# Optimization experiments

Hardware: AMD Instinct MI355X
Metric: run time of the kernel (lower is better)

The kernel has to match this reference:

```python
import jax, jax.numpy as jnp
import numpy as np

N, D, R, NUM_HEADS = 8192, 256, 32, 4
ETA = 0.5


def setup_inputs() -> dict:
    key = jax.random.key(0)
    k_h, k_a, k_u = jax.random.split(key, 3)
    H = jax.random.normal(k_h, (N, D), dtype=jnp.float32)
    # sparse-ish symmetric adjacency with self loops (float mask, as in torch code)
    A = (jax.random.uniform(k_a, (N, N)) < 0.002).astype(jnp.float32)
    A = jnp.maximum(jnp.maximum(A, A.T), jnp.eye(N, dtype=jnp.float32))
    # symmetric normalized Laplacian L = I - D^{-1/2} A D^{-1/2}
    dinv = 1.0 / jnp.sqrt(A.sum(axis=1))
    L = jnp.eye(N, dtype=jnp.float32) - dinv[:, None] * A * dinv[None, :]
    # per-head orthonormal subspace bases U[k] in R^{D x R} (QR init as in module)
    raw = jax.random.normal(k_u, (NUM_HEADS, D, R), dtype=jnp.float32)
    U = jnp.linalg.qr(raw)[0]  # batched reduced QR -> [K, D, R]
    lambda_lap = jnp.asarray(0.1, dtype=jnp.float32)
    threshold = jnp.full((D,), 0.05, dtype=jnp.float32)
    return {"H": H, "adj_mask": A, "L": L, "U": U,
            "lambda_lap": lambda_lap, "threshold": threshold}


def reference(H, adj_mask, L, U, lambda_lap, threshold):
    n, d = H.shape
    K, _, r = U.shape
    scale = 1.0 / (r ** 0.5)
    neg = (1.0 - adj_mask) * -1e9  # additive graph mask, shared across heads

    Ht = H.T  # [d, n]
    agg = jnp.zeros_like(Ht)
    for k in range(K):  # small fixed head loop (keeps one [n,n] block live at a time)
        Uk = U[k]                      # [d, r]
        Zk = Uk.T @ Ht                 # [r, n]
        scores = (Zk.T @ Zk) * scale + neg  # [n, n]
        alpha = jax.nn.softmax(scores, axis=1)
        agg = agg + Uk @ (Zk @ alpha.T)     # [d, n]

    lap_grad = lambda_lap * (L @ H)        # [n, d]
    H_half = (Ht + ETA * agg).T - ETA * lap_grad
    # proximal soft-threshold (proj is None since in_dim == out_dim)
    H_out = jnp.sign(H_half) * jax.nn.relu(jnp.abs(H_half) - threshold[None, :])

    # orthogonality regularizer over all head pairs
    G = jnp.einsum('kdr,lds->klrs', U, U)  # [K, K, r, r] (small)
    I = jnp.eye(r, dtype=U.dtype)
    diag_loss = ((G[jnp.arange(K), jnp.arange(K)] - I) ** 2).sum()
    upper = jnp.triu(jnp.ones((K, K), dtype=U.dtype), 1)
    off_loss = ((G ** 2).sum(axis=(2, 3)) * upper).sum()
    orth_loss = diag_loss + off_loss

    lap_smooth = jnp.sum(H_out * (L @ H_out))  # trace(H_out^T L H_out)
    return H_out, orth_loss, lap_smooth
```

## Files before the change

### kernel.cpp

```cpp
#include <hip/hip_runtime.h>
#include <hip/hip_bf16.h>
#include <math.h>

#define NN 8192
#define DD 256
#define RR 32
#define KH 4
#define PP 128
#define CAP 128
#define CAPL 128
#define NSTASH 48
#define ETA 0.5f
#define SCALE 0.17677669529663687f

__device__ __forceinline__ unsigned short f2bf(float f) {
  union { float f; unsigned u; } v; v.f = f;
  unsigned r = v.u + 0x7fffu + ((v.u >> 16) & 1u);
  return (unsigned short)(r >> 16);
}
__device__ __forceinline__ float bflo(unsigned u) { return __uint_as_float(u << 16); }
__device__ __forceinline__ float bfhi(unsigned u) { return __uint_as_float(u & 0xffff0000u); }

__global__ __launch_bounds__(256) void zgemm_scan(const float* __restrict__ A,
                                                  const float* __restrict__ H,
                                                  const float* __restrict__ U,
                                                  float* __restrict__ B2,
                                                  unsigned short* __restrict__ Zb,
                                                  unsigned short* __restrict__ Hb,
                                                  float* __restrict__ orth_part,
                                                  int* __restrict__ lowCols,
                                                  int* __restrict__ lowCnt,
                                                  int* __restrict__ upCols,
                                                  int* __restrict__ upCnt) {
  __shared__ float smem[5152];
  int tid = threadIdx.x;
  int bx = blockIdx.x;
  int lane = tid & 63, wv = tid >> 6;

  if (bx >= 650) {
    int row = (NN - 1) - (bx - 650);
    const float* a = A + (size_t)row * NN;
    __shared__ int wsum2[4];
    __shared__ int sbase;
    if (tid == 0) sbase = 0;
    int nch = (row >> 10) + 1;
    for (int c = 0; c < nch; ++c) {
      int g0 = c * 1024 + tid * 4;
      float4 x = *(const float4*)(a + g0);
      int m0 = (g0 + 0 < row) && (x.x != 0.f);
      int m1 = (g0 + 1 < row) && (x.y != 0.f);
      int m2 = (g0 + 2 < row) && (x.z != 0.f);
      int m3 = (g0 + 3 < row) && (x.w != 0.f);
      int cnt = m0 + m1 + m2 + m3;
      int incl = cnt;
#pragma unroll
      for (int off = 1; off < 64; off <<= 1) {
        int t = __shfl_up(incl, off);
        if (lane >= off) incl += t;
      }
      if (lane == 63) wsum2[wv] = incl;
      __syncthreads();
      int base = sbase;
#pragma unroll
      for (int w = 0; w < 4; ++w) if (w < wv) base += wsum2[w];
      int o = base + incl - cnt;
      int chunkTot = wsum2[0] + wsum2[1] + wsum2[2] + wsum2[3];
      if (m0) { int col = g0 + 0; if (o < CAPL) { lowCols[(size_t)row * CAPL + o] = col; int s = atomicAdd(&upCnt[col], 1); if (s < CAPL) upCols[(size_t)col * CAPL + s] = row; } o++; }
      if (m1) { int col = g0 + 1; if (o < CAPL) { lowCols[(size_t)row * CAPL + o] = col; int s = atomicAdd(&upCnt[col], 1); if (s < CAPL) upCols[(size_t)col * CAPL + s] = row; } o++; }
      if (m2) { int col = g0 + 2; if (o < CAPL) { lowCols[(size_t)row * CAPL + o] = col; int s = atomicAdd(&upCnt[col], 1); if (s < CAPL) upCols[(size_t)col * CAPL + s] = row; } o++; }
      if (m3) { int col = g0 + 3; if (o < CAPL) { lowCols[(size_t)row * CAPL + o] = col; int s = atomicAdd(&upCnt[col], 1); if (s < CAPL) upCols[(size_t)col * CAPL + s] = row; } o++; }
      __syncthreads();
      if (tid == 0) sbase = base + chunkTot;
    }
    __syncthreads();
    if (tid == 0) lowCnt[row] = sbase;
    return;
  }
  if (bx >= 394) {
    int base = (bx - 394) * 8192;
#pragma unroll
    for (int q = 0; q < 8; ++q) {
      int idx = base + q * 1024 + tid * 4;
      float4 v = *(const float4*)(H + idx);
      uint2 p;
      p.x = (unsigned)f2bf(v.x) | ((unsigned)f2bf(v.y) << 16);
      p.y = (unsigned)f2bf(v.z) | ((unsigned)f2bf(v.w) << 16);
      *(uint2*)(Hb + idx) = p;
    }
    return;
  }
  if (bx >= 266) {
    int idx = (bx - 266) * 256 + tid;
    int k = idx / (DD * RR);
    int rem = idx % (DD * RR);
    int d = rem / RR;
    int r = rem % RR;
    B2[(k * RR + r) * DD + d] = U[idx];
    return;
  }
  if (bx >= 256) {
    int bid = bx - 256;
    int b = bid, k = 0;
    while (b >= (KH - k)) { b -= (KH - k); k++; }
    int l = k + b;
    float* redo = smem;
    const float* uk = U + (size_t)k * DD * RR;
    const float* ul = U + (size_t)l * DD * RR;
    float acc = 0.f;
#pragma unroll
    for (int q = 0; q < 4; ++q) {
      int e = tid * 4 + q;
      int r = e >> 5, s2 = e & 31;
      float g = 0.f;
      for (int d = 0; d < DD; ++d) g += uk[d * RR + r] * ul[d * RR + s2];
      if (k == l) {
        float c3 = g - (r == s2 ? 1.f : 0.f);
        acc += c3 * c3;
      } else {
        acc += g * g;
      }
    }
    redo[tid] = acc;
    __syncthreads();
    for (int off = 128; off > 0; off >>= 1) {
      if (tid < off) redo[tid] += redo[tid + off];
      __syncthreads();
    }
    if (tid == 0) orth_part[bid] = redo[0];
    return;
  }
  float* As = smem;
  float* Bs = smem + 1056;
  int r0 = bx * 32;
  int tx = tid & 15, ty = tid >> 4;
  int cx = tx * 8, ry = ty * 2;
  float acc[2][8];
#pragma unroll
  for (int i = 0; i < 2; ++i)
#pragma unroll
    for (int j = 0; j < 8; ++j) acc[i][j] = 0.f;

  for (int k0 = 0; k0 < DD; k0 += 32) {
    {
      int r = tid >> 3;
      int kc = (tid & 7) * 4;
      float4 x = *(const float4*)(H + (size_t)(r0 + r) * DD + k0 + kc);
      As[(kc + 0) * 33 + r] = x.x; As[(kc + 1) * 33 + r] = x.y;
      As[(kc + 2) * 33 + r] = x.z; As[(kc + 3) * 33 + r] = x.w;
    }
#pragma unroll
    for (int q = 0; q < 4; ++q) {
      int f = tid + 256 * q;
      int kk = f >> 5, pc = (f & 31) * 4;
      *(float4*)(&Bs[kk * 128 + pc]) =
          *(const float4*)(U + (size_t)(pc >> 5) * DD * RR + (size_t)(k0 + kk) * RR + (pc & 31));
    }
    __syncthreads();
#pragma unroll
    for (int kk = 0; kk < 32; ++kk) {
      float av[2];
      av[0] = As[kk * 33 + ry]; av[1] = As[kk * 33 + ry + 1];
      float bv[8];
      *(float4*)(bv) = *(const float4*)(&Bs[kk * 128 + cx]);
      *(float4*)(bv + 4) = *(const float4*)(&Bs[kk * 128 + cx + 4]);
#pragma unroll
      for (int i = 0; i < 2; ++i)
#pragma unroll
        for (int j = 0; j < 8; ++j) acc[i][j] += av[i] * bv[j];
    }
    __syncthreads();
  }
#pragma unroll
  for (int i = 0; i < 2; ++i) {
    uint4 p;
    p.x = (unsigned)f2bf(acc[i][0]) | ((unsigned)f2bf(acc[i][1]) << 16);
    p.y = (unsigned)f2bf(acc[i][2]) | ((unsigned)f2bf(acc[i][3]) << 16);
    p.z = (unsigned)f2bf(acc[i][4]) | ((unsigned)f2bf(acc[i][5]) << 16);
    p.w = (unsigned)f2bf(acc[i][6]) | ((unsigned)f2bf(acc[i][7]) << 16);
    *(uint4*)(Zb + (size_t)(r0 + ry + i) * PP + cx) = p;
  }
}

__global__ __launch_bounds__(256) void csr_attn_s(const unsigned short* __restrict__ Zb,
                                                  const unsigned short* __restrict__ Hb,
                                                  const int* __restrict__ lowCols,
                                                  const int* __restrict__ lowCnt,
                                                  const int* __restrict__ upCols,
                                                  const int* __restrict__ upCnt,
                                                  float* __restrict__ dinv,
                                                  float* __restrict__ aggZ,
                                                  float* __restrict__ S) {
  int row = blockIdx.x;
  int tid = threadIdx.x;
  int lane = tid & 63, wv = tid >> 6;
  __shared__ int scols[CAP];
  __shared__ int utmp[CAPL];
  __shared__ float zi[PP];
  __shared__ unsigned short zzb[NSTASH][130];
  __shared__ float sdinv[CAP];
  __shared__ float uni[1024];

  if (tid < PP) zi[tid] = bflo((unsigned)Zb[(size_t)row * PP + tid]);

  int lcT = lowCnt[row];
  int ucT = upCnt[row];
  int lc = lcT < (CAP - 1) ? lcT : (CAP - 1);
  for (int t = tid; t < lc; t += 256) scols[t] = lowCols[(size_t)row * CAPL + t];
  if (tid == 0) scols[lc] = row;
  int ucR = ucT < CAPL ? ucT : CAPL;
  for (int t = tid; t < ucR; t += 256) utmp[t] = upCols[(size_t)row * CAPL + t];
  __syncthreads();
  for (int t = tid; t < ucR; t += 256) {
    int e = utmp[t], r = 0;
    for (int q = 0; q < ucR; ++q) r += (utmp[q] < e);
    int pos = lc + 1 + r;
    if (pos < CAP) scols[pos] = e;
  }
  int total = lcT + 1 + ucT;
  int nn = total < CAP ? total : CAP;
  if (tid == 0) dinv[row] = 1.0f / sqrtf((float)total);
  __syncthreads();

  if (tid < nn) {
    int c = scols[tid];
    int cc = lowCnt[c] + 1 + upCnt[c];
    sdinv[tid] = 1.0f / sqrtf((float)cc);
  }
  __syncthreads();

  {
    float4 acc = make_float4(0.f, 0.f, 0.f, 0.f);
    for (int jj = wv; jj < nn; jj += 4) {
      int c = scols[jj];
      if (jj < NSTASH) {
        unsigned x = *(const unsigned*)(Zb + (size_t)c * PP + lane * 2);
        *(unsigned*)(&zzb[jj][lane * 2]) = x;
      }
      uint2 u = *(const uint2*)(Hb + (size_t)c * DD + lane * 4);
      float w = sdinv[jj];
      acc.x += w * bflo(u.x); acc.y += w * bfhi(u.x);
      acc.z += w * bflo(u.y); acc.w += w * bfhi(u.y);
    }
    *(float4*)(&uni[wv * 256 + lane * 4]) = acc;
  }
  __syncthreads();
  {
    float s = uni[0 * 256 + tid] + uni[1 * 256 + tid] + uni[2 * 256 + tid] + uni[3 * 256 + tid];
    S[(size_t)row * DD + tid] = s;
  }
  __syncthreads();

  {
    int k = wv;
    float s0 = -1e30f, s1 = -1e30f;
    if (lane < nn) {
      float acc = 0.f;
      if (lane < NSTASH) {
        const unsigned short* zs = &zzb[lane][k * RR];
#pragma unroll
        for (int r = 0; r < RR; r += 4) {
          float4 aa = *(const float4*)(zi + k * RR + r);
          unsigned u0 = *(const unsigned*)(zs + r);
          unsigned u1 = *(const unsigned*)(zs + r + 2);
          acc += aa.x * bflo(u0) + aa.y * bfhi(u0) + aa.z * bflo(u1) + aa.w * bfhi(u1);
        }
      } else {
        const unsigned short* zj = Zb + (size_t)scols[lane] * PP + k * RR;
#pragma unroll
        for (int r = 0; r < RR; r += 4) {
          float4 aa = *(const float4*)(zi + k * RR + r);
          unsigned u0 = *(const unsigned*)(zj + r);
          unsigned u1 = *(const unsigned*)(zj + r + 2);
          acc += aa.x * bflo(u0) + aa.y * bfhi(u0) + aa.z * bflo(u1) + aa.w * bfhi(u1);
        }
      }
      s0 = acc * SCALE;
    }
    int j1 = lane + 64;
    if (j1 < nn) {
      const unsigned short* zj = Zb + (size_t)scols[j1] * PP + k * RR;
      float acc = 0.f;
#pragma unroll
      for (int r = 0; r < RR; r += 4) {
        float4 aa = *(const float4*)(zi + k * RR + r);
        unsigned u0 = *(const unsigned*)(zj + r);
        unsigned u1 = *(const unsigned*)(zj + r + 2);
        acc += aa.x * bflo(u0) + aa.y * bfhi(u0) + aa.z * bflo(u1) + aa.w * bfhi(u1);
      }
      s1 = acc * SCALE;
    }
    float m = fmaxf(s0, s1);
#pragma unroll
    for (int off = 32; off > 0; off >>= 1) m = fmaxf(m, __shfl_xor(m, off));
    float e0 = (lane < nn) ? expf(s0 - m) : 0.f;
    float e1 = (j1 < nn) ? expf(s1 - m) : 0.f;
    float s = e0 + e1;
#pragma unroll
    for (int off = 32; off > 0; off >>= 1) s += __shfl_xor(s, off);
    float inv = 1.0f / s;
    if (lane < nn) uni[k * CAP + lane] = e0 * inv;
    if (j1 < nn) uni[k * CAP + j1] = e1 * inv;
  }
  __syncthreads();

  {
    int c2 = tid & 63, hf = tid >> 6;
    int hd = c2 >> 4;
    float a0 = 0.f, a1 = 0.f;
    for (int jj = hf; jj < nn; jj += 4) {
      unsigned u;
      if (jj < NSTASH) u = *(const unsigned*)(&zzb[jj][c2 * 2]);
      else u = *(const unsigned*)(Zb + (size_t)scols[jj] * PP + c2 * 2);
      float al = uni[hd * CAP + jj];
      a0 += al * bflo(u);
      a1 += al * bfhi(u);
    }
    *(float2*)(&uni[512 + hf * 128 + c2 * 2]) = make_float2(a0, a1);
  }
  __syncthreads();
  if (tid < 64) {
    float2 r0 = *(float2*)(&uni[512 + 0 * 128 + tid * 2]);
    float2 r1 = *(float2*)(&uni[512 + 1 * 128 + tid * 2]);
    float2 r2 = *(float2*)(&uni[512 + 2 * 128 + tid * 2]);
    float2 r3 = *(float2*)(&uni[512 + 3 * 128 + tid * 2]);
    float2 s2 = make_float2(r0.x + r1.x + r2.x + r3.x, r0.y + r1.y + r2.y + r3.y);
    *(float2*)(aggZ + (size_t)row * PP + tid * 2) = s2;
  }
}

__global__ __launch_bounds__(256) void egemm(const float* __restrict__ A,
                                             const float* __restrict__ B,
                                             const float* __restrict__ Hm,
                                             const float* __restrict__ S,
                                             const float* __restrict__ dinv,
                                             const float* __restrict__ thr,
                                             const float* __restrict__ lambda_p,
                                             float* __restrict__ out,
                                             unsigned short* __restrict__ Houtb) {
  __shared__ float As[32][33];
  __shared__ float Bs[32][128];
  int tid = threadIdx.x;
  int r0 = blockIdx.x * 32;
  int c0 = blockIdx.y * 128;
  int tx = tid & 15, ty = tid >> 4;
  int cx = tx * 8, ry = ty * 2;
  float acc[2][8];
#pragma unroll
  for (int i = 0; i < 2; ++i)
#pragma unroll
    for (int j = 0; j < 8; ++j) acc[i][j] = 0.f;

  for (int k0 = 0; k0 < PP; k0 += 32) {
    {
      int r = tid >> 3;
      int kc = (tid & 7) * 4;
      float4 x = *(const float4*)(A + (size_t)(r0 + r) * PP + k0 + kc);
      As[kc + 0][r] = x.x; As[kc + 1][r] = x.y; As[kc + 2][r] = x.z; As[kc + 3][r] = x.w;
    }
#pragma unroll
    for (int q = 0; q < 4; ++q) {
      int f = tid + 256 * q;
      int kk = f >> 5, pc = (f & 31) * 4;
      *(float4*)(&Bs[kk][pc]) = *(const float4*)(B + (size_t)(k0 + kk) * DD + c0 + pc);
    }
    __syncthreads();
#pragma unroll
    for (int kk = 0; kk < 32; ++kk) {
      float av[2];
      av[0] = As[kk][ry]; av[1] = As[kk][ry + 1];
      float bv[8];
      *(float4*)(bv) = *(const float4*)(&Bs[kk][cx]);
      *(float4*)(bv + 4) = *(const float4*)(&Bs[kk][cx + 4]);
#pragma unroll
      for (int i = 0; i < 2; ++i)
#pragma unroll
        for (int j = 0; j < 8; ++j) acc[i][j] += av[i] * bv[j];
    }
    __syncthreads();
  }
  float lam = lambda_p[0];
  int gc = c0 + cx;
  float4 t0 = *(const float4*)(thr + gc);
  float4 t1 = *(const float4*)(thr + gc + 4);
#pragma unroll
  for (int i = 0; i < 2; ++i) {
    int gr = r0 + ry + i;
    float dv = dinv[gr];
    float4 h0 = *(const float4*)(Hm + (size_t)gr * DD + gc);
    float4 h1 = *(const float4*)(Hm + (size_t)gr * DD + gc + 4);
    float4 s0 = *(const float4*)(S + (size_t)gr * DD + gc);
    float4 s1 = *(const float4*)(S + (size_t)gr * DD + gc + 4);
    float hv[8] = {h0.x, h0.y, h0.z, h0.w, h1.x, h1.y, h1.z, h1.w};
    float sv[8] = {s0.x, s0.y, s0.z, s0.w, s1.x, s1.y, s1.z, s1.w};
    float tv[8] = {t0.x, t0.y, t0.z, t0.w, t1.x, t1.y, t1.z, t1.w};
    float ov[8];
#pragma unroll
    for (int j = 0; j < 8; ++j) {
      float val = hv[j] + ETA * acc[i][j] - ETA * lam * (hv[j] - dv * sv[j]);
      float av = fabsf(val) - tv[j];
      ov[j] = (av > 0.f) ? copysignf(av, val) : 0.f;
    }
    *(float4*)(out + (size_t)gr * DD + gc) = make_float4(ov[0], ov[1], ov[2], ov[3]);
    *(float4*)(out + (size_t)gr * DD + gc + 4) = make_float4(ov[4], ov[5], ov[6], ov[7]);
    uint4 p;
    p.x = (unsigned)f2bf(ov[0]) | ((unsigned)f2bf(ov[1]) << 16);
    p.y = (unsigned)f2bf(ov[2]) | ((unsigned)f2bf(ov[3]) << 16);
    p.z = (unsigned)f2bf(ov[4]) | ((unsigned)f2bf(ov[5]) << 16);
    p.w = (unsigned)f2bf(ov[6]) | ((unsigned)f2bf(ov[7]) << 16);
    *(uint4*)(Houtb + (size_t)gr * DD + gc) = p;
  }
}

__global__ __launch_bounds__(256) void lap_rows(const float* __restrict__ Hout,
                                                const unsigned short* __restrict__ Houtb,
                                                const int* __restrict__ lowCols,
                                                const int* __restrict__ lowCnt,
                                                const float* __restrict__ dinv,
                                                float* __restrict__ part) {
  int row = (NN - 1) - blockIdx.x;
  int tid = threadIdx.x;
  int lane = tid & 63, wv = tid >> 6;
  __shared__ int scols[CAPL];
  __shared__ float sdinv[CAPL];
  __shared__ float sred[4][260];
  int lcT = lowCnt[row];
  int lc = lcT < CAPL ? lcT : CAPL;
  if (tid < lc) {
    int c = lowCols[(size_t)row * CAPL + tid];
    scols[tid] = c;
    sdinv[tid] = 2.0f * dinv[c];
  }
  __syncthreads();
  float4 acc = make_float4(0.f, 0.f, 0.f, 0.f);
  for (int jj = wv; jj < lc; jj += 4) {
    uint2 u = *(const uint2*)(Houtb + (size_t)scols[jj] * DD + lane * 4);
    float w = sdinv[jj];
    acc.x += w * bflo(u.x); acc.y += w * bfhi(u.x);
    acc.z += w * bflo(u.y); acc.w += w * bfhi(u.y);
  }
  *(float4*)(&sred[wv][lane * 4]) = acc;
  __syncthreads();
  if (wv == 0) {
    float4 s4;
    s4.x = sred[0][lane * 4 + 0] + sred[1][lane * 4 + 0] + sred[2][lane * 4 + 0] + sred[3][lane * 4 + 0];
    s4.y = sred[0][lane * 4 + 1] + sred[1][lane * 4 + 1] + sred[2][lane * 4 + 1] + sred[3][lane * 4 + 1];
    s4.z = sred[0][lane * 4 + 2] + sred[1][lane * 4 + 2] + sred[2][lane * 4 + 2] + sred[3][lane * 4 + 2];
    s4.w = sred[0][lane * 4 + 3] + sred[1][lane * 4 + 3] + sred[2][lane * 4 + 3] + sred[3][lane * 4 + 3];
    float4 h4 = *(const float4*)(Hout + (size_t)row * DD + lane * 4);
    float dvr = dinv[row];
    float own = 1.0f - dvr * dvr;
    float val = h4.x * (own * h4.x - dvr * s4.x) + h4.y * (own * h4.y - dvr * s4.y) +
                h4.z * (own * h4.z - dvr * s4.z) + h4.w * (own * h4.w - dvr * s4.w);
#pragma unroll
    for (int off = 32; off > 0; off >>= 1) val += __shfl_xor(val, off);
    if (lane == 0) part[row] = val;
  }
}

__global__ __launch_bounds__(256) void finalize(const float* __restrict__ lap_part,
                                                const float* __restrict__ orth_part,
                                                float* __restrict__ out) {
  __shared__ double red[256];
  int tid = threadIdx.x;
  double s = 0.0;
  for (int i = tid; i < NN; i += 256) s += (double)lap_part[i];
  red[tid] = s;
  __syncthreads();
  for (int off = 128; off > 0; off >>= 1) {
    if (tid < off) red[tid] += red[tid + off];
    __syncthreads();
  }
  if (tid == 0) {
    double o = 0.0;
    for (int i = 0; i < 10; ++i) o += (double)orth_part[i];
    out[(size_t)NN * DD] = (float)o;
    out[(size_t)NN * DD + 1] = (float)red[0];
  }
}

extern "C" void kernel_launch(void* const* d_in, const int* in_sizes, int n_in,
                              void* d_out, int out_size, void* d_ws, size_t ws_size,
                              hipStream_t stream) {
  const float* H = (const float*)d_in[0];
  const float* A = (const float*)d_in[1];
  const float* U = (const float*)d_in[3];
  const float* lambda_p = (const float*)d_in[4];
  const float* thr = (const float*)d_in[5];
  float* out = (float*)d_out;

  char* w = (char*)d_ws;
  float* B2 = (float*)w;             w += (size_t)PP * DD * 4;
  int* lowCols = (int*)w;            w += (size_t)NN * CAPL * 4;
  int* upCols = (int*)w;             w += (size_t)NN * CAPL * 4;
  int* lowCnt = (int*)w;             w += (size_t)NN * 4;
  int* upCnt = (int*)w;              w += (size_t)NN * 4;
  float* dinv = (float*)w;           w += (size_t)NN * 4;
  unsigned short* Zb = (unsigned short*)w;   w += (size_t)NN * PP * 2;
  unsigned short* Hb = (unsigned short*)w;   w += (size_t)NN * DD * 2;
  unsigned short* Houtb = (unsigned short*)w; w += (size_t)NN * DD * 2;
  float* aggZ = (float*)w;           w += (size_t)NN * PP * 4;
  float* S = (float*)w;              w += (size_t)NN * DD * 4;
  float* lap_part = (float*)w;       w += (size_t)NN * 4;
  float* orth_part = (float*)w;      w += 64;

  hipMemsetAsync(upCnt, 0, (size_t)NN * 4, stream);
  zgemm_scan<<<dim3(650 + NN), dim3(256), 0, stream>>>(A, H, U, B2, Zb, Hb, orth_part,
                                                       lowCols, lowCnt, upCols, upCnt);
  csr_attn_s<<<dim3(NN), dim3(256), 0, stream>>>(Zb, Hb, lowCols, lowCnt, upCols, upCnt,
                                                 dinv, aggZ, S);
  egemm<<<dim3(NN / 32, 2), dim3(256), 0, stream>>>(aggZ, B2, H, S, dinv, thr, lambda_p,
                                                    out, Houtb);
  lap_rows<<<dim3(NN), dim3(256), 0, stream>>>(out, Houtb, lowCols, lowCnt, dinv, lap_part);
  finalize<<<dim3(1), dim3(256), 0, stream>>>(lap_part, orth_part, out);
}
```

Measured before the change: 152.6 us.

## Fuse sparse Laplacian gather into epilogue GEMM, drop S intermediate

The weighted neighbor sum of bf16 H (the L@H term) moves out of the attention kernel and into the egemm kernel. The attention kernel now writes a compact per-row column list and nnz count, and egemm gathers each 32-row by 128-column tile into shared memory before its GEMM loop. This removes the full-size fp32 S buffer write and re-read. In exchange, the gather now runs in a grid of only 512 blocks issuing small 4-byte loads, so latency may be less well hidden, and a new cols array is written.

```diff
diff --git a/kernel.cpp b/kernel.cpp
--- a/kernel.cpp
+++ b/kernel.cpp
@@ -181,15 +181,15 @@
   }
 }
 
-__global__ __launch_bounds__(256) void csr_attn_s(const unsigned short* __restrict__ Zb,
-                                                  const unsigned short* __restrict__ Hb,
-                                                  const int* __restrict__ lowCols,
-                                                  const int* __restrict__ lowCnt,
-                                                  const int* __restrict__ upCols,
-                                                  const int* __restrict__ upCnt,
-                                                  float* __restrict__ dinv,
-                                                  float* __restrict__ aggZ,
-                                                  float* __restrict__ S) {
+__global__ __launch_bounds__(256) void csr_attn(const unsigned short* __restrict__ Zb,
+                                                const int* __restrict__ lowCols,
+                                                const int* __restrict__ lowCnt,
+                                                const int* __restrict__ upCols,
+                                                const int* __restrict__ upCnt,
+                                                int* __restrict__ cols,
+                                                int* __restrict__ nnzArr,
+                                                float* __restrict__ dinv,
+                                                float* __restrict__ aggZ) {
   int row = blockIdx.x;
   int tid = threadIdx.x;
   int lane = tid & 63, wv = tid >> 6;
@@ -197,7 +197,6 @@
   __shared__ int utmp[CAPL];
   __shared__ float zi[PP];
   __shared__ unsigned short zzb[NSTASH][130];
-  __shared__ float sdinv[CAP];
   __shared__ float uni[1024];
 
   if (tid < PP) zi[tid] = bflo((unsigned)Zb[(size_t)row * PP + tid]);
@@ -219,34 +218,14 @@
   int total = lcT + 1 + ucT;
   int nn = total < CAP ? total : CAP;
   if (tid == 0) dinv[row] = 1.0f / sqrtf((float)total);
-  __syncthreads();
-
-  if (tid < nn) {
-    int c = scols[tid];
-    int cc = lowCnt[c] + 1 + upCnt[c];
-    sdinv[tid] = 1.0f / sqrtf((float)cc);
-  }
-  __syncthreads();
-
-  {
-    float4 acc = make_float4(0.f, 0.f, 0.f, 0.f);
-    for (int jj = wv; jj < nn; jj += 4) {
-      int c = scols[jj];
-      if (jj < NSTASH) {
-        unsigned x = *(const unsigned*)(Zb + (size_t)c * PP + lane * 2);
-        *(unsigned*)(&zzb[jj][lane * 2]) = x;
-      }
-      uint2 u = *(const uint2*)(Hb + (size_t)c * DD + lane * 4);
-      float w = sdinv[jj];
-      acc.x += w * bflo(u.x); acc.y += w * bfhi(u.x);
-      acc.z += w * bflo(u.y); acc.w += w * bfhi(u.y);
-    }
-    *(float4*)(&uni[wv * 256 + lane * 4]) = acc;
-  }
-  __syncthreads();
-  {
-    float s = uni[0 * 256 + tid] + uni[1 * 256 + tid] + uni[2 * 256 + tid] + uni[3 * 256 + tid];
-    S[(size_t)row * DD + tid] = s;
+  if (tid == 0) nnzArr[row] = nn;
+  __syncthreads();
+  for (int t = tid; t < nn; t += 256) cols[(size_t)row * CAP + t] = scols[t];
+
+  int ns = nn < NSTASH ? nn : NSTASH;
+  for (int j = wv; j < ns; j += 4) {
+    unsigned x = *(const unsigned*)(Zb + (size_t)scols[j] * PP + lane * 2);
+    *(unsigned*)(&zzb[j][lane * 2]) = x;
   }
   __syncthreads();
 
@@ -331,7 +310,9 @@
 __global__ __launch_bounds__(256) void egemm(const float* __restrict__ A,
                                              const float* __restrict__ B,
                                              const float* __restrict__ Hm,
-                                             const float* __restrict__ S,
+                                             const unsigned short* __restrict__ Hb,
+                                             const int* __restrict__ cols,
+                                             const int* __restrict__ nnzArr,
                                              const float* __restrict__ dinv,
                                              const float* __restrict__ thr,
                                              const float* __restrict__ lambda_p,
@@ -339,11 +320,38 @@
                                              unsigned short* __restrict__ Houtb) {
   __shared__ float As[32][33];
   __shared__ float Bs[32][128];
+  __shared__ float Stile[32][130];
   int tid = threadIdx.x;
+  int lane = tid & 63, wv = tid >> 6;
   int r0 = blockIdx.x * 32;
   int c0 = blockIdx.y * 128;
   int tx = tid & 15, ty = tid >> 4;
   int cx = tx * 8, ry = ty * 2;
+
+  for (int r = wv; r < 32; r += 4) {
+    int gr = r0 + r;
+    int nn = nnzArr[gr];
+    const int* cp = cols + (size_t)gr * CAP;
+    float a0 = 0.f, a1 = 0.f, b0 = 0.f, b1 = 0.f;
+    int jj = 0;
+    for (; jj + 1 < nn; jj += 2) {
+      int ca = cp[jj], cb = cp[jj + 1];
+      float wa = dinv[ca], wb = dinv[cb];
+      unsigned ua = *(const unsigned*)(Hb + (size_t)ca * DD + c0 + lane * 2);
+      unsigned ub = *(const unsigned*)(Hb + (size_t)cb * DD + c0 + lane * 2);
+      a0 += wa * bflo(ua); a1 += wa * bfhi(ua);
+      b0 += wb * bflo(ub); b1 += wb * bfhi(ub);
+    }
+    if (jj < nn) {
+      int ca = cp[jj];
+      float wa = dinv[ca];
+      unsigned ua = *(const unsigned*)(Hb + (size_t)ca * DD + c0 + lane * 2);
+      a0 += wa * bflo(ua); a1 += wa * bfhi(ua);
+    }
+    Stile[r][lane * 2] = a0 + b0;
+    Stile[r][lane * 2 + 1] = a1 + b1;
+  }
+
   float acc[2][8];
 #pragma unroll
   for (int i = 0; i < 2; ++i)
@@ -378,6 +386,7 @@
     }
     __syncthreads();
   }
+
   float lam = lambda_p[0];
   int gc = c0 + cx;
   float4 t0 = *(const float4*)(thr + gc);
@@ -388,15 +397,13 @@
     float dv = dinv[gr];
     float4 h0 = *(const float4*)(Hm + (size_t)gr * DD + gc);
     float4 h1 = *(const float4*)(Hm + (size_t)gr * DD + gc + 4);
-    float4 s0 = *(const float4*)(S + (size_t)gr * DD + gc);
-    float4 s1 = *(const float4*)(S + (size_t)gr * DD + gc + 4);
     float hv[8] = {h0.x, h0.y, h0.z, h0.w, h1.x, h1.y, h1.z, h1.w};
-    float sv[8] = {s0.x, s0.y, s0.z, s0.w, s1.x, s1.y, s1.z, s1.w};
     float tv[8] = {t0.x, t0.y, t0.z, t0.w, t1.x, t1.y, t1.z, t1.w};
     float ov[8];
 #pragma unroll
     for (int j = 0; j < 8; ++j) {
-      float val = hv[j] + ETA * acc[i][j] - ETA * lam * (hv[j] - dv * sv[j]);
+      float sv = Stile[ry + i][cx + j];
+      float val = hv[j] + ETA * acc[i][j] - ETA * lam * (hv[j] - dv * sv);
       float av = fabsf(val) - tv[j];
       ov[j] = (av > 0.f) ? copysignf(av, val) : 0.f;
     }
@@ -492,24 +499,25 @@
   float* B2 = (float*)w;             w += (size_t)PP * DD * 4;
   int* lowCols = (int*)w;            w += (size_t)NN * CAPL * 4;
   int* upCols = (int*)w;             w += (size_t)NN * CAPL * 4;
+  int* cols = (int*)w;               w += (size_t)NN * CAP * 4;
   int* lowCnt = (int*)w;             w += (size_t)NN * 4;
   int* upCnt = (int*)w;              w += (size_t)NN * 4;
+  int* nnzArr = (int*)w;             w += (size_t)NN * 4;
   float* dinv = (float*)w;           w += (size_t)NN * 4;
   unsigned short* Zb = (unsigned short*)w;   w += (size_t)NN * PP * 2;
   unsigned short* Hb = (unsigned short*)w;   w += (size_t)NN * DD * 2;
   unsigned short* Houtb = (unsigned short*)w; w += (size_t)NN * DD * 2;
   float* aggZ = (float*)w;           w += (size_t)NN * PP * 4;
-  float* S = (float*)w;              w += (size_t)NN * DD * 4;
   float* lap_part = (float*)w;       w += (size_t)NN * 4;
   float* orth_part = (float*)w;      w += 64;
 
   hipMemsetAsync(upCnt, 0, (size_t)NN * 4, stream);
   zgemm_scan<<<dim3(650 + NN), dim3(256), 0, stream>>>(A, H, U, B2, Zb, Hb, orth_part,
                                                        lowCols, lowCnt, upCols, upCnt);
-  csr_attn_s<<<dim3(NN), dim3(256), 0, stream>>>(Zb, Hb, lowCols, lowCnt, upCols, upCnt,
-                                                 dinv, aggZ, S);
-  egemm<<<dim3(NN / 32, 2), dim3(256), 0, stream>>>(aggZ, B2, H, S, dinv, thr, lambda_p,
-                                                    out, Houtb);
+  csr_attn<<<dim3(NN), dim3(256), 0, stream>>>(Zb, lowCols, lowCnt, upCols, upCnt,
+                                               cols, nnzArr, dinv, aggZ);
+  egemm<<<dim3(NN / 32, 2), dim3(256), 0, stream>>>(aggZ, B2, H, Hb, cols, nnzArr, dinv,
+                                                    thr, lambda_p, out, Houtb);
   lap_rows<<<dim3(NN), dim3(256), 0, stream>>>(out, Houtb, lowCols, lowCnt, dinv, lap_part);
   finalize<<<dim3(1), dim3(256), 0, stream>>>(lap_part, orth_part, out);
 }
```

Result: slower. 197.1 us (+29.1%).

## Fuse output GEMM and epilogue into per-row sparse attention kernel

Applied to the files above, without the earlier changes.

Removes the separate egemm kernel. Each row block of the attention kernel now multiplies its aggregated Z vector by a bf16 copy of the U basis (B2b) and applies the Laplacian-gradient and soft-threshold epilogue itself. This avoids writing and re-reading the aggZ and S intermediates and saves a kernel launch. In exchange, each block re-reads the 64KB bf16 basis from cache as a per-row matrix-vector product, and U is now rounded to bf16.

```diff
diff --git a/kernel.cpp b/kernel.cpp
--- a/kernel.cpp
+++ b/kernel.cpp
@@ -24,7 +24,7 @@
 __global__ __launch_bounds__(256) void zgemm_scan(const float* __restrict__ A,
                                                   const float* __restrict__ H,
                                                   const float* __restrict__ U,
-                                                  float* __restrict__ B2,
+                                                  unsigned short* __restrict__ B2b,
                                                   unsigned short* __restrict__ Zb,
                                                   unsigned short* __restrict__ Hb,
                                                   float* __restrict__ orth_part,
@@ -95,7 +95,7 @@
     int rem = idx % (DD * RR);
     int d = rem / RR;
     int r = rem % RR;
-    B2[(k * RR + r) * DD + d] = U[idx];
+    B2b[(k * RR + r) * DD + d] = f2bf(U[idx]);
     return;
   }
   if (bx >= 256) {
@@ -181,15 +181,19 @@
   }
 }
 
-__global__ __launch_bounds__(256) void csr_attn_s(const unsigned short* __restrict__ Zb,
-                                                  const unsigned short* __restrict__ Hb,
-                                                  const int* __restrict__ lowCols,
-                                                  const int* __restrict__ lowCnt,
-                                                  const int* __restrict__ upCols,
-                                                  const int* __restrict__ upCnt,
-                                                  float* __restrict__ dinv,
-                                                  float* __restrict__ aggZ,
-                                                  float* __restrict__ S) {
+__global__ __launch_bounds__(256) void csr_attn_full(const unsigned short* __restrict__ Zb,
+                                                     const unsigned short* __restrict__ Hb,
+                                                     const unsigned short* __restrict__ B2b,
+                                                     const float* __restrict__ Hm,
+                                                     const float* __restrict__ thr,
+                                                     const float* __restrict__ lambda_p,
+                                                     const int* __restrict__ lowCols,
+                                                     const int* __restrict__ lowCnt,
+                                                     const int* __restrict__ upCols,
+                                                     const int* __restrict__ upCnt,
+                                                     float* __restrict__ dinv,
+                                                     float* __restrict__ out,
+                                                     unsigned short* __restrict__ Houtb) {
   int row = blockIdx.x;
   int tid = threadIdx.x;
   int lane = tid & 63, wv = tid >> 6;
@@ -218,7 +222,8 @@
   }
   int total = lcT + 1 + ucT;
   int nn = total < CAP ? total : CAP;
-  if (tid == 0) dinv[row] = 1.0f / sqrtf((float)total);
+  float dvRow = 1.0f / sqrtf((float)total);
+  if (tid == 0) dinv[row] = dvRow;
   __syncthreads();
 
   if (tid < nn) {
@@ -244,10 +249,7 @@
     *(float4*)(&uni[wv * 256 + lane * 4]) = acc;
   }
   __syncthreads();
-  {
-    float s = uni[0 * 256 + tid] + uni[1 * 256 + tid] + uni[2 * 256 + tid] + uni[3 * 256 + tid];
-    S[(size_t)row * DD + tid] = s;
-  }
+  float sReg = uni[0 * 256 + tid] + uni[1 * 256 + tid] + uni[2 * 256 + tid] + uni[3 * 256 + tid];
   __syncthreads();
 
   {
@@ -323,91 +325,37 @@
     float2 r1 = *(float2*)(&uni[512 + 1 * 128 + tid * 2]);
     float2 r2 = *(float2*)(&uni[512 + 2 * 128 + tid * 2]);
     float2 r3 = *(float2*)(&uni[512 + 3 * 128 + tid * 2]);
-    float2 s2 = make_float2(r0.x + r1.x + r2.x + r3.x, r0.y + r1.y + r2.y + r3.y);
-    *(float2*)(aggZ + (size_t)row * PP + tid * 2) = s2;
-  }
-}
-
-__global__ __launch_bounds__(256) void egemm(const float* __restrict__ A,
-                                             const float* __restrict__ B,
-                                             const float* __restrict__ Hm,
-                                             const float* __restrict__ S,
-                                             const float* __restrict__ dinv,
-                                             const float* __restrict__ thr,
-                                             const float* __restrict__ lambda_p,
-                                             float* __restrict__ out,
-                                             unsigned short* __restrict__ Houtb) {
-  __shared__ float As[32][33];
-  __shared__ float Bs[32][128];
-  int tid = threadIdx.x;
-  int r0 = blockIdx.x * 32;
-  int c0 = blockIdx.y * 128;
-  int tx = tid & 15, ty = tid >> 4;
-  int cx = tx * 8, ry = ty * 2;
-  float acc[2][8];
-#pragma unroll
-  for (int i = 0; i < 2; ++i)
-#pragma unroll
-    for (int j = 0; j < 8; ++j) acc[i][j] = 0.f;
-
-  for (int k0 = 0; k0 < PP; k0 += 32) {
-    {
-      int r = tid >> 3;
-      int kc = (tid & 7) * 4;
-      float4 x = *(const float4*)(A + (size_t)(r0 + r) * PP + k0 + kc);
-      As[kc + 0][r] = x.x; As[kc + 1][r] = x.y; As[kc + 2][r] = x.z; As[kc + 3][r] = x.w;
-    }
-#pragma unroll
-    for (int q = 0; q < 4; ++q) {
-      int f = tid + 256 * q;
-      int kk = f >> 5, pc = (f & 31) * 4;
-      *(float4*)(&Bs[kk][pc]) = *(const float4*)(B + (size_t)(k0 + kk) * DD + c0 + pc);
-    }
-    __syncthreads();
-#pragma unroll
-    for (int kk = 0; kk < 32; ++kk) {
-      float av[2];
-      av[0] = As[kk][ry]; av[1] = As[kk][ry + 1];
-      float bv[8];
-      *(float4*)(bv) = *(const float4*)(&Bs[kk][cx]);
-      *(float4*)(bv + 4) = *(const float4*)(&Bs[kk][cx + 4]);
-#pragma unroll
-      for (int i = 0; i < 2; ++i)
-#pragma unroll
-        for (int j = 0; j < 8; ++j) acc[i][j] += av[i] * bv[j];
-    }
-    __syncthreads();
-  }
-  float lam = lambda_p[0];
-  int gc = c0 + cx;
-  float4 t0 = *(const float4*)(thr + gc);
-  float4 t1 = *(const float4*)(thr + gc + 4);
-#pragma unroll
-  for (int i = 0; i < 2; ++i) {
-    int gr = r0 + ry + i;
-    float dv = dinv[gr];
-    float4 h0 = *(const float4*)(Hm + (size_t)gr * DD + gc);
-    float4 h1 = *(const float4*)(Hm + (size_t)gr * DD + gc + 4);
-    float4 s0 = *(const float4*)(S + (size_t)gr * DD + gc);
-    float4 s1 = *(const float4*)(S + (size_t)gr * DD + gc + 4);
-    float hv[8] = {h0.x, h0.y, h0.z, h0.w, h1.x, h1.y, h1.z, h1.w};
-    float sv[8] = {s0.x, s0.y, s0.z, s0.w, s1.x, s1.y, s1.z, s1.w};
-    float tv[8] = {t0.x, t0.y, t0.z, t0.w, t1.x, t1.y, t1.z, t1.w};
-    float ov[8];
-#pragma unroll
-    for (int j = 0; j < 8; ++j) {
-      float val = hv[j] + ETA * acc[i][j] - ETA * lam * (hv[j] - dv * sv[j]);
-      float av = fabsf(val) - tv[j];
-      ov[j] = (av > 0.f) ? copysignf(av, val) : 0.f;
-    }
-    *(float4*)(out + (size_t)gr * DD + gc) = make_float4(ov[0], ov[1], ov[2], ov[3]);
-    *(float4*)(out + (size_t)gr * DD + gc + 4) = make_float4(ov[4], ov[5], ov[6], ov[7]);
-    uint4 p;
-    p.x = (unsigned)f2bf(ov[0]) | ((unsigned)f2bf(ov[1]) << 16);
-    p.y = (unsigned)f2bf(ov[2]) | ((unsigned)f2bf(ov[3]) << 16);
-    p.z = (unsigned)f2bf(ov[4]) | ((unsigned)f2bf(ov[5]) << 16);
-    p.w = (unsigned)f2bf(ov[6]) | ((unsigned)f2bf(ov[7]) << 16);
-    *(uint4*)(Houtb + (size_t)gr * DD + gc) = p;
+    uni[tid * 2] = r0.x + r1.x + r2.x + r3.x;
+    uni[tid * 2 + 1] = r0.y + r1.y + r2.y + r3.y;
+  }
+  __syncthreads();
+
+  {
+    int g = tid >> 7, t = tid & 127;
+    float a0 = 0.f, a1 = 0.f;
+    int pbase = g * 64;
+#pragma unroll 8
+    for (int p = 0; p < 64; ++p) {
+      float az = uni[pbase + p];
+      unsigned u = *(const unsigned*)(B2b + (size_t)(pbase + p) * DD + t * 2);
+      a0 += az * bflo(u);
+      a1 += az * bfhi(u);
+    }
+    uni[512 + g * 256 + t * 2] = a0;
+    uni[512 + g * 256 + t * 2 + 1] = a1;
+  }
+  __syncthreads();
+
+  {
+    float agg = uni[512 + tid] + uni[768 + tid];
+    float h = Hm[(size_t)row * DD + tid];
+    float lam = lambda_p[0];
+    float t = thr[tid];
+    float val = h + ETA * agg - ETA * lam * (h - dvRow * sReg);
+    float av = fabsf(val) - t;
+    float ov = (av > 0.f) ? copysignf(av, val) : 0.f;
+    out[(size_t)row * DD + tid] = ov;
+    Houtb[(size_t)row * DD + tid] = f2bf(ov);
   }
 }
 
@@ -489,7 +437,7 @@
   float* out = (float*)d_out;
 
   char* w = (char*)d_ws;
-  float* B2 = (float*)w;             w += (size_t)PP * DD * 4;
+  unsigned short* B2b = (unsigned short*)w;  w += (size_t)PP * DD * 2;
   int* lowCols = (int*)w;            w += (size_t)NN * CAPL * 4;
   int* upCols = (int*)w;             w += (size_t)NN * CAPL * 4;
   int* lowCnt = (int*)w;             w += (size_t)NN * 4;
@@ -498,18 +446,15 @@
   unsigned short* Zb = (unsigned short*)w;   w += (size_t)NN * PP * 2;
   unsigned short* Hb = (unsigned short*)w;   w += (size_t)NN * DD * 2;
   unsigned short* Houtb = (unsigned short*)w; w += (size_t)NN * DD * 2;
-  float* aggZ = (float*)w;           w += (size_t)NN * PP * 4;
-  float* S = (float*)w;              w += (size_t)NN * DD * 4;
   float* lap_part = (float*)w;       w += (size_t)NN * 4;
   float* orth_part = (float*)w;      w += 64;
 
   hipMemsetAsync(upCnt, 0, (size_t)NN * 4, stream);
-  zgemm_scan<<<dim3(650 + NN), dim3(256), 0, stream>>>(A, H, U, B2, Zb, Hb, orth_part,
+  zgemm_scan<<<dim3(650 + NN), dim3(256), 0, stream>>>(A, H, U, B2b, Zb, Hb, orth_part,
                                                        lowCols, lowCnt, upCols, upCnt);
-  csr_attn_s<<<dim3(NN), dim3(256), 0, stream>>>(Zb, Hb, lowCols, lowCnt, upCols, upCnt,
-                                                 dinv, aggZ, S);
-  egemm<<<dim3(NN / 32, 2), dim3(256), 0, stream>>>(aggZ, B2, H, S, dinv, thr, lambda_p,
-                                                    out, Houtb);
+  csr_attn_full<<<dim3(NN), dim3(256), 0, stream>>>(Zb, Hb, B2b, H, thr, lambda_p,
+                                                    lowCols, lowCnt, upCols, upCnt,
+                                                    dinv, out, Houtb);
   lap_rows<<<dim3(NN), dim3(256), 0, stream>>>(out, Houtb, lowCols, lowCnt, dinv, lap_part);
   finalize<<<dim3(1), dim3(256), 0, stream>>>(lap_part, orth_part, out);
 }
```

After: 166.3 us. 1.09x slower.

## Pair triangular scan rows per block and unroll neighbor gathers for memory parallelism

Applied to the files above, without the earlier changes.

The lower-triangle adjacency scan now pairs row p with row N-1-p in a single block, so every block does about the same amount of work, and the launch uses half as many blocks. Each thread loads up to 32 contiguous floats in registers instead of looping over 1024-wide chunks with shared base carries, which removes the per-chunk barriers. The neighbor gather loops in csr_attn_s and lap_rows are unrolled by four with separate accumulators to keep more loads in flight. The cost is higher register pressure, and each thread's strided 128-byte segments may coalesce less well.

```diff
diff --git a/kernel.cpp b/kernel.cpp
--- a/kernel.cpp
+++ b/kernel.cpp
@@ -38,20 +38,26 @@
   int lane = tid & 63, wv = tid >> 6;
 
   if (bx >= 650) {
-    int row = (NN - 1) - (bx - 650);
-    const float* a = A + (size_t)row * NN;
+    int p = bx - 650;
     __shared__ int wsum2[4];
-    __shared__ int sbase;
-    if (tid == 0) sbase = 0;
-    int nch = (row >> 10) + 1;
-    for (int c = 0; c < nch; ++c) {
-      int g0 = c * 1024 + tid * 4;
-      float4 x = *(const float4*)(a + g0);
-      int m0 = (g0 + 0 < row) && (x.x != 0.f);
-      int m1 = (g0 + 1 < row) && (x.y != 0.f);
-      int m2 = (g0 + 2 < row) && (x.z != 0.f);
-      int m3 = (g0 + 3 < row) && (x.w != 0.f);
-      int cnt = m0 + m1 + m2 + m3;
+#pragma unroll
+    for (int half = 0; half < 2; ++half) {
+      int row = (half == 0) ? (NN - 1 - p) : p;
+      int limit = row;
+      int base0 = tid * 32;
+      const float* a = A + (size_t)row * NN + base0;
+      float4 v[8];
+      int cnt = 0;
+#pragma unroll
+      for (int c = 0; c < 8; ++c) {
+        if (base0 + c * 4 < limit) {
+          v[c] = *(const float4*)(a + c * 4);
+          cnt += (base0 + c * 4 + 0 < limit && v[c].x != 0.f);
+          cnt += (base0 + c * 4 + 1 < limit && v[c].y != 0.f);
+          cnt += (base0 + c * 4 + 2 < limit && v[c].z != 0.f);
+          cnt += (base0 + c * 4 + 3 < limit && v[c].w != 0.f);
+        }
+      }
       int incl = cnt;
 #pragma unroll
       for (int off = 1; off < 64; off <<= 1) {
@@ -60,20 +66,25 @@
       }
       if (lane == 63) wsum2[wv] = incl;
       __syncthreads();
-      int base = sbase;
+      int base = 0;
 #pragma unroll
       for (int w = 0; w < 4; ++w) if (w < wv) base += wsum2[w];
       int o = base + incl - cnt;
-      int chunkTot = wsum2[0] + wsum2[1] + wsum2[2] + wsum2[3];
-      if (m0) { int col = g0 + 0; if (o < CAPL) { lowCols[(size_t)row * CAPL + o] = col; int s = atomicAdd(&upCnt[col], 1); if (s < CAPL) upCols[(size_t)col * CAPL + s] = row; } o++; }
-      if (m1) { int col = g0 + 1; if (o < CAPL) { lowCols[(size_t)row * CAPL + o] = col; int s = atomicAdd(&upCnt[col], 1); if (s < CAPL) upCols[(size_t)col * CAPL + s] = row; } o++; }
-      if (m2) { int col = g0 + 2; if (o < CAPL) { lowCols[(size_t)row * CAPL + o] = col; int s = atomicAdd(&upCnt[col], 1); if (s < CAPL) upCols[(size_t)col * CAPL + s] = row; } o++; }
-      if (m3) { int col = g0 + 3; if (o < CAPL) { lowCols[(size_t)row * CAPL + o] = col; int s = atomicAdd(&upCnt[col], 1); if (s < CAPL) upCols[(size_t)col * CAPL + s] = row; } o++; }
+      int total = wsum2[0] + wsum2[1] + wsum2[2] + wsum2[3];
+#pragma unroll
+      for (int c = 0; c < 8; ++c) {
+        if (base0 + c * 4 < limit) {
+          float4 x = v[c];
+          int col = base0 + c * 4;
+          if (col + 0 < limit && x.x != 0.f) { if (o < CAPL) { lowCols[(size_t)row * CAPL + o] = col + 0; int s = atomicAdd(&upCnt[col + 0], 1); if (s < CAPL) upCols[(size_t)(col + 0) * CAPL + s] = row; } o++; }
+          if (col + 1 < limit && x.y != 0.f) { if (o < CAPL) { lowCols[(size_t)row * CAPL + o] = col + 1; int s = atomicAdd(&upCnt[col + 1], 1); if (s < CAPL) upCols[(size_t)(col + 1) * CAPL + s] = row; } o++; }
+          if (col + 2 < limit && x.z != 0.f) { if (o < CAPL) { lowCols[(size_t)row * CAPL + o] = col + 2; int s = atomicAdd(&upCnt[col + 2], 1); if (s < CAPL) upCols[(size_t)(col + 2) * CAPL + s] = row; } o++; }
+          if (col + 3 < limit && x.w != 0.f) { if (o < CAPL) { lowCols[(size_t)row * CAPL + o] = col + 3; int s = atomicAdd(&upCnt[col + 3], 1); if (s < CAPL) upCols[(size_t)(col + 3) * CAPL + s] = row; } o++; }
+        }
+      }
+      if (tid == 0) lowCnt[row] = total;
       __syncthreads();
-      if (tid == 0) sbase = base + chunkTot;
-    }
-    __syncthreads();
-    if (tid == 0) lowCnt[row] = sbase;
+    }
     return;
   }
   if (bx >= 394) {
@@ -82,10 +93,10 @@
     for (int q = 0; q < 8; ++q) {
       int idx = base + q * 1024 + tid * 4;
       float4 v = *(const float4*)(H + idx);
-      uint2 p;
-      p.x = (unsigned)f2bf(v.x) | ((unsigned)f2bf(v.y) << 16);
-      p.y = (unsigned)f2bf(v.z) | ((unsigned)f2bf(v.w) << 16);
-      *(uint2*)(Hb + idx) = p;
+      uint2 p2;
+      p2.x = (unsigned)f2bf(v.x) | ((unsigned)f2bf(v.y) << 16);
+      p2.y = (unsigned)f2bf(v.z) | ((unsigned)f2bf(v.w) << 16);
+      *(uint2*)(Hb + idx) = p2;
     }
     return;
   }
@@ -229,19 +240,62 @@
   __syncthreads();
 
   {
-    float4 acc = make_float4(0.f, 0.f, 0.f, 0.f);
-    for (int jj = wv; jj < nn; jj += 4) {
-      int c = scols[jj];
+    float4 a0 = make_float4(0.f, 0.f, 0.f, 0.f);
+    float4 a1 = make_float4(0.f, 0.f, 0.f, 0.f);
+    float4 a2 = make_float4(0.f, 0.f, 0.f, 0.f);
+    float4 a3 = make_float4(0.f, 0.f, 0.f, 0.f);
+    for (int jj = wv; jj < nn; jj += 16) {
+      int j1 = jj + 4, j2 = jj + 8, j3 = jj + 12;
+      bool b1 = j1 < nn, b2 = j2 < nn, b3 = j3 < nn;
+      int c0 = scols[jj];
+      int c1 = b1 ? scols[j1] : 0;
+      int c2 = b2 ? scols[j2] : 0;
+      int c3 = b3 ? scols[j3] : 0;
+      uint2 u0 = *(const uint2*)(Hb + (size_t)c0 * DD + lane * 4);
+      uint2 u1, u2, u3;
+      if (b1) u1 = *(const uint2*)(Hb + (size_t)c1 * DD + lane * 4);
+      if (b2) u2 = *(const uint2*)(Hb + (size_t)c2 * DD + lane * 4);
+      if (b3) u3 = *(const uint2*)(Hb + (size_t)c3 * DD + lane * 4);
       if (jj < NSTASH) {
-        unsigned x = *(const unsigned*)(Zb + (size_t)c * PP + lane * 2);
+        unsigned x = *(const unsigned*)(Zb + (size_t)c0 * PP + lane * 2);
         *(unsigned*)(&zzb[jj][lane * 2]) = x;
       }
-      uint2 u = *(const uint2*)(Hb + (size_t)c * DD + lane * 4);
-      float w = sdinv[jj];
-      acc.x += w * bflo(u.x); acc.y += w * bfhi(u.x);
-      acc.z += w * bflo(u.y); acc.w += w * bfhi(u.y);
-    }
-    *(float4*)(&uni[wv * 256 + lane * 4]) = acc;
+      if (b1 && j1 < NSTASH) {
+        unsigned x = *(const unsigned*)(Zb + (size_t)c1 * PP + lane * 2);
+        *(unsigned*)(&zzb[j1][lane * 2]) = x;
+      }
+      if (b2 && j2 < NSTASH) {
+        unsigned x = *(const unsigned*)(Zb + (size_t)c2 * PP + lane * 2);
+        *(unsigned*)(&zzb[j2][lane * 2]) = x;
+      }
+      if (b3 && j3 < NSTASH) {
+        unsigned x = *(const unsigned*)(Zb + (size_t)c3 * PP + lane * 2);
+        *(unsigned*)(&zzb[j3][lane * 2]) = x;
+      }
+      float w0 = sdinv[jj];
+      a0.x += w0 * bflo(u0.x); a0.y += w0 * bfhi(u0.x);
+      a0.z += w0 * bflo(u0.y); a0.w += w0 * bfhi(u0.y);
+      if (b1) {
+        float w1 = sdinv[j1];
+        a1.x += w1 * bflo(u1.x); a1.y += w1 * bfhi(u1.x);
+        a1.z += w1 * bflo(u1.y); a1.w += w1 * bfhi(u1.y);
+      }
+      if (b2) {
+        float w2 = sdinv[j2];
+        a2.x += w2 * bflo(u2.x); a2.y += w2 * bfhi(u2.x);
+        a2.z += w2 * bflo(u2.y); a2.w += w2 * bfhi(u2.y);
+      }
+      if (b3) {
+        float w3 = sdinv[j3];
+        a3.x += w3 * bflo(u3.x); a3.y += w3 * bfhi(u3.x);
+        a3.z += w3 * bflo(u3.y); a3.w += w3 * bfhi(u3.y);
+      }
+    }
+    a0.x += a1.x + a2.x + a3.x;
+    a0.y += a1.y + a2.y + a3.y;
+    a0.z += a1.z + a2.z + a3.z;
+    a0.w += a1.w + a2.w + a3.w;
+    *(float4*)(&uni[wv * 256 + lane * 4]) = a0;
   }
   __syncthreads();
   {
@@ -431,14 +485,42 @@
     sdinv[tid] = 2.0f * dinv[c];
   }
   __syncthreads();
-  float4 acc = make_float4(0.f, 0.f, 0.f, 0.f);
-  for (int jj = wv; jj < lc; jj += 4) {
-    uint2 u = *(const uint2*)(Houtb + (size_t)scols[jj] * DD + lane * 4);
-    float w = sdinv[jj];
-    acc.x += w * bflo(u.x); acc.y += w * bfhi(u.x);
-    acc.z += w * bflo(u.y); acc.w += w * bfhi(u.y);
-  }
-  *(float4*)(&sred[wv][lane * 4]) = acc;
+  float4 a0 = make_float4(0.f, 0.f, 0.f, 0.f);
+  float4 a1 = make_float4(0.f, 0.f, 0.f, 0.f);
+  float4 a2 = make_float4(0.f, 0.f, 0.f, 0.f);
+  float4 a3 = make_float4(0.f, 0.f, 0.f, 0.f);
+  for (int jj = wv; jj < lc; jj += 16) {
+    int j1 = jj + 4, j2 = jj + 8, j3 = jj + 12;
+    bool b1 = j1 < lc, b2 = j2 < lc, b3 = j3 < lc;
+    uint2 u0 = *(const uint2*)(Houtb + (size_t)scols[jj] * DD + lane * 4);
+    uint2 u1, u2, u3;
+    if (b1) u1 = *(const uint2*)(Houtb + (size_t)scols[j1] * DD + lane * 4);
+    if (b2) u2 = *(const uint2*)(Houtb + (size_t)scols[j2] * DD + lane * 4);
+    if (b3) u3 = *(const uint2*)(Houtb + (size_t)scols[j3] * DD + lane * 4);
+    float w0 = sdinv[jj];
+    a0.x += w0 * bflo(u0.x); a0.y += w0 * bfhi(u0.x);
+    a0.z += w0 * bflo(u0.y); a0.w += w0 * bfhi(u0.y);
+    if (b1) {
+      float w1 = sdinv[j1];
+      a1.x += w1 * bflo(u1.x); a1.y += w1 * bfhi(u1.x);
+      a1.z += w1 * bflo(u1.y); a1.w += w1 * bfhi(u1.y);
+    }
+    if (b2) {
+      float w2 = sdinv[j2];
+      a2.x += w2 * bflo(u2.x); a2.y += w2 * bfhi(u2.x);
+      a2.z += w2 * bflo(u2.y); a2.w += w2 * bfhi(u2.y);
+    }
+    if (b3) {
+      float w3 = sdinv[j3];
+      a3.x += w3 * bflo(u3.x); a3.y += w3 * bfhi(u3.x);
+      a3.z += w3 * bflo(u3.y); a3.w += w3 * bfhi(u3.y);
+    }
+  }
+  a0.x += a1.x + a2.x + a3.x;
+  a0.y += a1.y + a2.y + a3.y;
+  a0.z += a1.z + a2.z + a3.z;
+  a0.w += a1.w + a2.w + a3.w;
+  *(float4*)(&sred[wv][lane * 4]) = a0;
   __syncthreads();
   if (wv == 0) {
     float4 s4;
@@ -504,8 +586,8 @@
   float* orth_part = (float*)w;      w += 64;
 
   hipMemsetAsync(upCnt, 0, (size_t)NN * 4, stream);
-  zgemm_scan<<<dim3(650 + NN), dim3(256), 0, stream>>>(A, H, U, B2, Zb, Hb, orth_part,
-                                                       lowCols, lowCnt, upCols, upCnt);
+  zgemm_scan<<<dim3(650 + NN / 2), dim3(256), 0, stream>>>(A, H, U, B2, Zb, Hb, orth_part,
+                                                           lowCols, lowCnt, upCols, upCnt);
   csr_attn_s<<<dim3(NN), dim3(256), 0, stream>>>(Zb, Hb, lowCols, lowCnt, upCols, upCnt,
                                                  dinv, aggZ, S);
   egemm<<<dim3(NN / 32, 2), dim3(256), 0, stream>>>(aggZ, B2, H, S, dinv, thr, lambda_p,
```

Result: slower. 163.5 us (+7.1%).
